# Performance work log

Measured on AMD Instinct MI355X. Metric: run time of the kernel, lower is better.

Reference implementation:

```python
import jax, jax.numpy as jnp
import numpy as np

N, S, H = 16, 2048, 1024
K = 8           # num_models (experts)
D = H // 4      # bottleneck = hidden_dim // ds_factor


def setup_inputs() -> dict:
    key = jax.random.key(0)
    k1, k2, k3, k4, k5, k6 = jax.random.split(key, 6)
    hidden_states = jax.random.normal(k1, (N, S, H), dtype=jnp.float32)
    p = jax.random.uniform(k2, (N, K), dtype=jnp.float32)
    prob = p / jnp.sum(p, axis=-1, keepdims=True)  # normalized routing probs
    std = 0.02
    w_down = jax.random.normal(k3, (K, D, H), dtype=jnp.float32) * std
    b_down = jax.random.normal(k4, (K, D), dtype=jnp.float32) * std
    w_up = jax.random.normal(k5, (K, H, D), dtype=jnp.float32) * std
    b_up = jax.random.normal(k6, (K, H), dtype=jnp.float32) * std
    return {"hidden_states": hidden_states, "prob": prob,
            "w_down": w_down, "b_down": b_down,
            "w_up": w_up, "b_up": b_up}


def merge_linear(x, prob, weight, bias):
    # weight: (K, out, in); prob: (N, K) -> per-instance merged weight (N, out, in)
    w = jnp.einsum('nk,koi->noi', prob, weight)
    b = jnp.einsum('nk,ko->no', prob, bias)
    # x: (N, S, in) -> (N, S, out); matmul with per-instance weight^T
    y = jnp.einsum('nsi,noi->nso', x, w)
    return y + b[:, None, :]


def reference(hidden_states, prob, w_down, b_down, w_up, b_up):
    # MergeAdapter forward (ln_before=False, ln_after=False, dropout=0)
    residual = merge_linear(hidden_states, prob, w_down, b_down)
    residual = jax.nn.relu(residual)
    residual = merge_linear(residual, prob, w_up, b_up)
    return hidden_states + residual
```

## Files before the change

kernel.cpp:

```cpp
#include <hip/hip_runtime.h>


typedef unsigned short u16;
typedef __bf16 bf16x8 __attribute__((ext_vector_type(8)));
typedef float f32x4 __attribute__((ext_vector_type(4)));

__device__ __forceinline__ u16 f2bf(float f) {
    union { float f; unsigned int i; } v; v.f = f;
    unsigned int r = v.i + 0x7fffu + ((v.i >> 16) & 1u);
    return (u16)(r >> 16);
}

__device__ __forceinline__ void gload_lds16(const u16* g, u16* l) {
    __builtin_amdgcn_global_load_lds(
        (const __attribute__((address_space(1))) void*)g,
        (__attribute__((address_space(3))) void*)l,
        16, 0, 0);
}

__device__ __forceinline__ void store8(u16* dst, float4 a, float4 b) {
    union { uint4 u; u16 s[8]; } cv;
    cv.s[0]=f2bf(a.x); cv.s[1]=f2bf(a.y); cv.s[2]=f2bf(a.z); cv.s[3]=f2bf(a.w);
    cv.s[4]=f2bf(b.x); cv.s[5]=f2bf(b.y); cv.s[6]=f2bf(b.z); cv.s[7]=f2bf(b.w);
    *(uint4*)dst = cv.u;
}

__global__ __launch_bounds__(256)
void merge_kernel(const float* __restrict__ prob,
                  const float* __restrict__ w_down, const float* __restrict__ b_down,
                  const float* __restrict__ w_up,   const float* __restrict__ b_up,
                  u16* __restrict__ Wd, u16* __restrict__ Wu,
                  float* __restrict__ bd, float* __restrict__ bu)
{
    __shared__ float sp[128];
    const int tid = threadIdx.x;
    if (tid < 128) sp[tid] = prob[tid];
    __syncthreads();

    const int bid = blockIdx.x;
    const int E = 256 * 1024;

    if (bid < 256) {
        int v = bid * 256 + tid;
        const bool down = (v < 32768);
        const int vv = down ? v : (v - 32768);
        const float* W = down ? w_down : w_up;
        u16* O = down ? Wd : Wu;
        const size_t e = (size_t)vv * 8;

        float wf[8][8];
        #pragma unroll
        for (int k = 0; k < 8; ++k) {
            const float4 f0 = *(const float4*)(W + (size_t)k * E + e);
            const float4 f1 = *(const float4*)(W + (size_t)k * E + e + 4);
            wf[k][0] = f0.x; wf[k][1] = f0.y; wf[k][2] = f0.z; wf[k][3] = f0.w;
            wf[k][4] = f1.x; wf[k][5] = f1.y; wf[k][6] = f1.z; wf[k][7] = f1.w;
        }
        for (int n = 0; n < 16; ++n) {
            float a[8] = {0.f,0.f,0.f,0.f,0.f,0.f,0.f,0.f};
            #pragma unroll
            for (int k = 0; k < 8; ++k) {
                const float p = sp[n * 8 + k];
                #pragma unroll
                for (int j = 0; j < 8; ++j) a[j] = fmaf(p, wf[k][j], a[j]);
            }
            union { uint4 u; u16 s[8]; } ov;
            #pragma unroll
            for (int j = 0; j < 8; ++j) ov.s[j] = f2bf(a[j]);
            *(uint4*)(O + (size_t)n * E + e) = ov.u;
        }
    } else {
        int idx = (bid - 256) * 256 + tid;
        if (idx < 16 * 256) {
            const int n = idx >> 8, d = idx & 255;
            float s = 0.f;
            #pragma unroll
            for (int k = 0; k < 8; ++k)
                s = fmaf(sp[n * 8 + k], b_down[k * 256 + d], s);
            bd[idx] = s;
        } else {
            const int i2 = idx - 4096;
            const int n = i2 >> 10, h = i2 & 1023;
            float s = 0.f;
            #pragma unroll
            for (int k = 0; k < 8; ++k)
                s = fmaf(sp[n * 8 + k], b_up[k * 1024 + h], s);
            bu[i2] = s;
        }
    }
}

__global__ __launch_bounds__(512, 2)
void fused_adapter(const float* __restrict__ x, const u16* __restrict__ Wd,
                   const u16* __restrict__ Wu, const float* __restrict__ bd,
                   const float* __restrict__ bu, float* __restrict__ out)
{
    __shared__ __align__(16) u16 lds0[32768];
    __shared__ __align__(16) u16 lds1[32768];

    const int tid  = threadIdx.x;
    const int lane = tid & 63;
    const int wave = tid >> 6;
    const int quad = lane >> 4, rl = lane & 15;
    const int rxl  = rl & 7;

    const int id = blockIdx.x;
    const int r4 = id & 15;
    const int batch = (r4 & 7) * 2 + (r4 >> 3);
    const int mblk  = id >> 4;

    const float* xb  = x  + (size_t)batch * 2048 * 1024 + (size_t)mblk * 128 * 1024;
    const u16*   Wdb = Wd + (size_t)batch * 256 * 1024;
    const u16*   Wub = Wu + (size_t)batch * 1024 * 256;
    const float* bdb = bd + batch * 256;
    const float* bub = bu + batch * 1024;
    float*       ob  = out + (size_t)batch * 2048 * 1024 + (size_t)mblk * 128 * 1024;

    const int wm1 = wave >> 2, wn1 = wave & 3;

    u16* const b0x = lds1;  u16* const b0w = lds1 + 8192;
    u16* const b1x = lds0;  u16* const b1w = lds0 + 8192;

    const int xrow = tid >> 3, xsl = tid & 7;
    const int xdst0 = (xrow * 8 + (xsl ^ (xrow & 7))) * 8;
    const int xdst1 = xdst0 + 4096;
    const int wrow  = tid >> 3;
    const int wgcol = ((tid & 7) ^ ((tid >> 3) & 7)) * 8;

    f32x4 acc1[4][4] = {};

    {
        const float4 a0 = *(const float4*)(xb + (size_t)xrow * 1024 + xsl * 8);
        const float4 a1 = *(const float4*)(xb + (size_t)xrow * 1024 + xsl * 8 + 4);
        const float4 a2 = *(const float4*)(xb + (size_t)(xrow + 64) * 1024 + xsl * 8);
        const float4 a3 = *(const float4*)(xb + (size_t)(xrow + 64) * 1024 + xsl * 8 + 4);
        #pragma unroll
        for (int r = 0; r < 4; ++r)
            gload_lds16(Wdb + (size_t)(r * 64 + wrow) * 1024 + wgcol,
                        b0w + (size_t)(r * 512 + wave * 64) * 8);
        store8(b0x + xdst0, a0, a1);
        store8(b0x + xdst1, a2, a3);
    }
    __syncthreads();

    for (int it = 0; it < 16; ++it) {
        u16* cx = (it & 1) ? b1x : b0x;
        u16* cw = (it & 1) ? b1w : b0w;
        u16* nx = (it & 1) ? b0x : b1x;
        u16* nw = (it & 1) ? b0w : b1w;
        const int k1 = (it + 1) * 64;

        float4 a0, a1, a2, a3;
        if (it < 15) {
            a0 = *(const float4*)(xb + (size_t)xrow * 1024 + k1 + xsl * 8);
            a1 = *(const float4*)(xb + (size_t)xrow * 1024 + k1 + xsl * 8 + 4);
            a2 = *(const float4*)(xb + (size_t)(xrow + 64) * 1024 + k1 + xsl * 8);
            a3 = *(const float4*)(xb + (size_t)(xrow + 64) * 1024 + k1 + xsl * 8 + 4);
            #pragma unroll
            for (int r = 0; r < 4; ++r)
                gload_lds16(Wdb + (size_t)(r * 64 + wrow) * 1024 + k1 + wgcol,
                            nw + (size_t)(r * 512 + wave * 64) * 8);
        }

        #pragma unroll
        for (int kk = 0; kk < 64; kk += 32) {
            bf16x8 av[4], bv[4];
            #pragma unroll
            for (int mi = 0; mi < 4; ++mi)
                av[mi] = *(const bf16x8*)(cx + (wm1 * 64 + mi * 16 + rl) * 64
                                          + ((kk / 8 + quad) ^ rxl) * 8);
            #pragma unroll
            for (int ni = 0; ni < 4; ++ni)
                bv[ni] = *(const bf16x8*)(cw + (wn1 * 64 + ni * 16 + rl) * 64
                                          + ((kk / 8 + quad) ^ rxl) * 8);
            #pragma unroll
            for (int mi = 0; mi < 4; ++mi)
                #pragma unroll
                for (int ni = 0; ni < 4; ++ni)
                    acc1[mi][ni] = __builtin_amdgcn_mfma_f32_16x16x32_bf16(
                        av[mi], bv[ni], acc1[mi][ni], 0, 0, 0);
        }

        if (it < 15) { store8(nx + xdst0, a0, a1); store8(nx + xdst1, a2, a3); }
        __syncthreads();
    }

    #pragma unroll
    for (int ni = 0; ni < 4; ++ni) {
        const int col = wn1 * 64 + ni * 16 + rl;
        const float bv = bdb[col];
        const int lbc = col >> 3, hi = lbc & 24, c7 = lbc & 7, cl = col & 7;
        #pragma unroll
        for (int mi = 0; mi < 4; ++mi)
            #pragma unroll
            for (int i = 0; i < 4; ++i) {
                const int row = wm1 * 64 + mi * 16 + quad * 4 + i;
                const int phys = hi | (c7 ^ (row & 7));
                lds0[row * 256 + phys * 8 + cl] =
                    f2bf(fmaxf(acc1[mi][ni][i] + bv, 0.0f));
            }
    }
    __syncthreads();

    const int wm2 = wave >> 2, wn2 = wave & 3;

    const int srow = tid >> 5, ss = tid & 31;
    const int wugcol = ((ss & 24) | ((ss & 7) ^ (srow & 7))) * 8;

    auto stage_wu = [&](int c, u16* buf) {
        #pragma unroll
        for (int rr = 0; rr < 8; ++rr)
            gload_lds16(Wub + (size_t)(c * 128 + rr * 16 + srow) * 256 + wugcol,
                        buf + (size_t)(rr * 512 + wave * 64) * 8);
    };

    stage_wu(0, lds1);

    bf16x8 af[4][8];
    #pragma unroll
    for (int mi = 0; mi < 4; ++mi) {
        const int rowb = (wm2 * 64 + mi * 16 + rl) * 256;
        #pragma unroll
        for (int t = 0; t < 8; ++t) {
            const int lb = t * 4 + quad;
            const int phys = (lb & 24) | ((lb & 7) ^ rxl);
            af[mi][t] = *(const bf16x8*)(lds0 + rowb + phys * 8);
        }
    }
    __syncthreads();

    u16* cur = lds1;
    u16* nxt = lds0;
    for (int c = 0; c < 8; ++c) {
        if (c < 7) stage_wu(c + 1, nxt);

        f32x4 acc2[4][2] = {};
        #pragma unroll
        for (int t = 0; t < 8; ++t) {
            bf16x8 bv[2];
            #pragma unroll
            for (int ni = 0; ni < 2; ++ni) {
                const int rowb = (wn2 * 32 + ni * 16 + rl) * 256;
                const int lb = t * 4 + quad;
                const int phys = (lb & 24) | ((lb & 7) ^ rxl);
                bv[ni] = *(const bf16x8*)(cur + rowb + phys * 8);
            }
            #pragma unroll
            for (int mi = 0; mi < 4; ++mi)
                #pragma unroll
                for (int ni = 0; ni < 2; ++ni)
                    acc2[mi][ni] = __builtin_amdgcn_mfma_f32_16x16x32_bf16(
                        af[mi][t], bv[ni], acc2[mi][ni], 0, 0, 0);
        }

        #pragma unroll
        for (int ni = 0; ni < 2; ++ni) {
            const int colg = c * 128 + wn2 * 32 + ni * 16 + rl;
            const float bv = bub[colg];
            #pragma unroll
            for (int mi = 0; mi < 4; ++mi)
                #pragma unroll
                for (int i = 0; i < 4; ++i) {
                    const int rowl = wm2 * 64 + mi * 16 + quad * 4 + i;
                    const size_t off = (size_t)rowl * 1024 + colg;
                    ob[off] = acc2[mi][ni][i] + bv + xb[off];
                }
        }

        if (c < 7) {
            u16* t2 = cur; cur = nxt; nxt = t2;
            __syncthreads();
        }
    }
}

extern "C" void kernel_launch(void* const* d_in, const int* in_sizes, int n_in,
                              void* d_out, int out_size, void* d_ws, size_t ws_size,
                              hipStream_t stream) {
    const float* hidden = (const float*)d_in[0];
    const float* prob   = (const float*)d_in[1];
    const float* w_down = (const float*)d_in[2];
    const float* b_down = (const float*)d_in[3];
    const float* w_up   = (const float*)d_in[4];
    const float* b_up   = (const float*)d_in[5];
    float* out = (float*)d_out;

    u16* Wd = (u16*)d_ws;
    u16* Wu = Wd + (size_t)16 * 256 * 1024;
    float* bd = (float*)(Wu + (size_t)16 * 1024 * 256);
    float* bu = bd + 16 * 256;

    merge_kernel<<<336, 256, 0, stream>>>(prob, w_down, b_down, w_up, b_up,
                                          Wd, Wu, bd, bu);

    fused_adapter<<<256, 512, 0, stream>>>(hidden, Wd, Wu, bd, bu, out);
}
```

Before: 329.0 us.

## Load up-projection weights directly from global memory instead of LDS staging

The second GEMM stage no longer double-buffers W_up chunks into LDS with global_load_lds and barriers. Instead each wave owns a contiguous slice of 256 output columns and reads its B fragments straight from global memory, looping over 16 narrow column chunks. It also prefetches the residual x values before the MFMAs so the loads overlap with compute. This removes the per-chunk __syncthreads and LDS traffic, but each wave now reads uncoalesced 16-byte fragments from global or L2, and the output stores become narrower per chunk.

```diff
diff --git a/kernel.cpp b/kernel.cpp
--- a/kernel.cpp
+++ b/kernel.cpp
@@ -204,18 +204,6 @@
 
     const int wm2 = wave >> 2, wn2 = wave & 3;
 
-    const int srow = tid >> 5, ss = tid & 31;
-    const int wugcol = ((ss & 24) | ((ss & 7) ^ (srow & 7))) * 8;
-
-    auto stage_wu = [&](int c, u16* buf) {
-        #pragma unroll
-        for (int rr = 0; rr < 8; ++rr)
-            gload_lds16(Wub + (size_t)(c * 128 + rr * 16 + srow) * 256 + wugcol,
-                        buf + (size_t)(rr * 512 + wave * 64) * 8);
-    };
-
-    stage_wu(0, lds1);
-
     bf16x8 af[4][8];
     #pragma unroll
     for (int mi = 0; mi < 4; ++mi) {
@@ -227,50 +215,43 @@
             af[mi][t] = *(const bf16x8*)(lds0 + rowb + phys * 8);
         }
     }
-    __syncthreads();
-
-    u16* cur = lds1;
-    u16* nxt = lds0;
-    for (int c = 0; c < 8; ++c) {
-        if (c < 7) stage_wu(c + 1, nxt);
-
-        f32x4 acc2[4][2] = {};
-        #pragma unroll
-        for (int t = 0; t < 8; ++t) {
-            bf16x8 bv[2];
-            #pragma unroll
-            for (int ni = 0; ni < 2; ++ni) {
-                const int rowb = (wn2 * 32 + ni * 16 + rl) * 256;
-                const int lb = t * 4 + quad;
-                const int phys = (lb & 24) | ((lb & 7) ^ rxl);
-                bv[ni] = *(const bf16x8*)(cur + rowb + phys * 8);
+
+    const u16* Wuw = Wub + (size_t)(wn2 * 256) * 256;
+
+    for (int c = 0; c < 16; ++c) {
+        const int col0 = c * 16;
+        const int colg = wn2 * 256 + col0 + rl;
+
+        bf16x8 bv[8];
+        #pragma unroll
+        for (int t = 0; t < 8; ++t)
+            bv[t] = *(const bf16x8*)(Wuw + (size_t)(col0 + rl) * 256
+                                     + t * 32 + quad * 8);
+
+        float xr[4][4];
+        #pragma unroll
+        for (int mi = 0; mi < 4; ++mi)
+            #pragma unroll
+            for (int i = 0; i < 4; ++i)
+                xr[mi][i] = xb[(size_t)(wm2 * 64 + mi * 16 + quad * 4 + i) * 1024
+                               + colg];
+
+        f32x4 acc2[4] = {};
+        #pragma unroll
+        for (int t = 0; t < 8; ++t)
+            #pragma unroll
+            for (int mi = 0; mi < 4; ++mi)
+                acc2[mi] = __builtin_amdgcn_mfma_f32_16x16x32_bf16(
+                    af[mi][t], bv[t], acc2[mi], 0, 0, 0);
+
+        const float buv = bub[colg];
+        #pragma unroll
+        for (int mi = 0; mi < 4; ++mi)
+            #pragma unroll
+            for (int i = 0; i < 4; ++i) {
+                const int row = wm2 * 64 + mi * 16 + quad * 4 + i;
+                ob[(size_t)row * 1024 + colg] = acc2[mi][i] + buv + xr[mi][i];
             }
-            #pragma unroll
-            for (int mi = 0; mi < 4; ++mi)
-                #pragma unroll
-                for (int ni = 0; ni < 2; ++ni)
-                    acc2[mi][ni] = __builtin_amdgcn_mfma_f32_16x16x32_bf16(
-                        af[mi][t], bv[ni], acc2[mi][ni], 0, 0, 0);
-        }
-
-        #pragma unroll
-        for (int ni = 0; ni < 2; ++ni) {
-            const int colg = c * 128 + wn2 * 32 + ni * 16 + rl;
-            const float bv = bub[colg];
-            #pragma unroll
-            for (int mi = 0; mi < 4; ++mi)
-                #pragma unroll
-                for (int i = 0; i < 4; ++i) {
-                    const int rowl = wm2 * 64 + mi * 16 + quad * 4 + i;
-                    const size_t off = (size_t)rowl * 1024 + colg;
-                    ob[off] = acc2[mi][ni][i] + bv + xb[off];
-                }
-        }
-
-        if (c < 7) {
-            u16* t2 = cur; cur = nxt; nxt = t2;
-            __syncthreads();
-        }
     }
 }
 
```

Measured after the change: 354.0 us. +7.6%, slower.
